# Kernel tuning notes

Hardware: AMD Instinct MI355X
Metric: run time of the kernel (lower is better)

Reference implementation:

```python
import jax, jax.numpy as jnp
import numpy as np

B, C, L, H, D = 2, 1024, 2048, 16, 64  # batch, n_factor, seq, heads, head_dim
LN_EPS = 1e-5


def setup_inputs() -> dict:
    key = jax.random.key(0)
    ks = jax.random.split(key, 8)
    s = 0.02
    return {
        "x": jax.random.normal(ks[0], (B, C, L), jnp.float32),
        "y": jax.random.normal(ks[1], (B, C, L), jnp.float32),
        "Wq": jax.random.normal(ks[2], (H, C, D), jnp.float32) * s,
        "Wk": jax.random.normal(ks[3], (H, C, D), jnp.float32) * s,
        "Wv": jax.random.normal(ks[4], (H, C, D), jnp.float32) * s,
        "bq": jax.random.normal(ks[5], (H, D), jnp.float32) * s,
        "bk": jax.random.normal(ks[6], (H, D), jnp.float32) * s,
        "bv": jax.random.normal(ks[7], (H, D), jnp.float32) * s,
        "gamma": jnp.ones((C,), jnp.float32),
        "beta": jnp.zeros((C,), jnp.float32),
    }


def reference(x, y, Wq, Wk, Wv, bq, bk, bv, gamma, beta):
    # Per-head Conv1d(kernel=1) == per-position linear; batch all heads at once.
    # x,y: [B, C, L]; W*: [H, C, D]; result q/k/v: [B, H, L, D]
    q = jnp.einsum('bcl,hcd->bhld', x, Wq) + bq[None, :, None, :]
    k = jnp.einsum('bcl,hcd->bhld', y, Wk) + bk[None, :, None, :]
    v = jnp.einsum('bcl,hcd->bhld', y, Wv) + bv[None, :, None, :]

    scale = 1.0 / jnp.sqrt(jnp.float32(D))  # n_factor_head ** 0.5
    scores = jnp.einsum('bhqd,bhkd->bhqk', q, k) * scale  # [B,H,L,L]
    attn = jax.nn.softmax(scores, axis=-1)
    ctx = jnp.einsum('bhqk,bhkd->bhqd', attn, v)  # [B,H,L,D]

    # torch.cat over heads along last dim == [B, L, H*D]
    att = jnp.transpose(ctx, (0, 2, 1, 3)).reshape(B, L, H * D)

    h = jnp.transpose(x, (0, 2, 1)) + att  # residual on x permuted to [B,L,C]
    mu = jnp.mean(h, axis=-1, keepdims=True)
    var = jnp.var(h, axis=-1, keepdims=True)
    out = (h - mu) * jax.lax.rsqrt(var + LN_EPS) * gamma + beta
    # dropout: identity in eval mode
    return out
```

## Files before the change

### kernel.cpp

```cpp
#include <hip/hip_runtime.h>
#include <hip/hip_bf16.h>

#define DEVI __device__ __forceinline__

typedef unsigned short u16;
typedef __bf16 bf16x8 __attribute__((ext_vector_type(8)));
typedef float f32x4 __attribute__((ext_vector_type(4)));

constexpr int Bn = 2, Cn = 1024, Ln = 2048, Hn = 16, Dn = 64;

DEVI u16 f2bfu(float f) { return __builtin_bit_cast(u16, __float2bfloat16(f)); }
DEVI float bfu2f(u16 u) { return __bfloat162float(__builtin_bit_cast(__hip_bfloat16, u)); }
DEVI f32x4 mfma16(bf16x8 a, bf16x8 b, f32x4 c) {
  return __builtin_amdgcn_mfma_f32_16x16x32_bf16(a, b, c, 0, 0, 0);
}
DEVI unsigned pk2(float lo, float hi) {
  return (unsigned)f2bfu(lo) | ((unsigned)f2bfu(hi) << 16);
}
DEVI void gld16(const u16* g, u16* l) {
  __builtin_amdgcn_global_load_lds(
      (const __attribute__((address_space(1))) unsigned*)g,
      (__attribute__((address_space(3))) unsigned*)l, 16, 0, 0);
}
DEVI int fsw(int row) { return (row & 7) ^ (((row >> 3) & 1) << 2); }

__global__ __launch_bounds__(256) void transpose_xy(const float* __restrict__ x,
                                                    const float* __restrict__ y,
                                                    u16* __restrict__ xT,
                                                    u16* __restrict__ yT) {
  int z = blockIdx.z;
  int which = z >> 1, b = z & 1;
  const float* src = (which ? y : x) + (size_t)b * Cn * Ln;
  u16* dst = (which ? yT : xT) + (size_t)b * Ln * Cn;
  int l0 = blockIdx.x * 64, c0 = blockIdx.y * 64;
  __shared__ float tile[64][65];
  int t = threadIdx.x;
  #pragma unroll
  for (int i = 0; i < 16; ++i) {
    int idx = i * 256 + t;
    int r = idx >> 6, cc = idx & 63;
    tile[r][cc] = src[(size_t)(c0 + r) * Ln + (l0 + cc)];
  }
  __syncthreads();
  #pragma unroll
  for (int i = 0; i < 8; ++i) {
    int idx = i * 256 + t;
    int r = idx >> 5, cc = (idx & 31) * 2;
    unsigned pkv = pk2(tile[cc][r], tile[cc + 1][r]);
    *(unsigned*)(&dst[(size_t)(l0 + r) * Cn + (c0 + cc)]) = pkv;
  }
}

__global__ __launch_bounds__(256) void transpose_w(const float* __restrict__ Wq,
                                                   const float* __restrict__ Wk,
                                                   const float* __restrict__ Wv,
                                                   u16* __restrict__ WT) {
  int c0 = blockIdx.x * 64, h = blockIdx.y, which = blockIdx.z;
  const float* src = (which == 0 ? Wq : (which == 1 ? Wk : Wv)) + (size_t)h * Cn * Dn;
  u16* dst = WT + ((size_t)which * Hn + h) * Dn * Cn;
  __shared__ float tile[64][65];
  int t = threadIdx.x;
  #pragma unroll
  for (int i = 0; i < 16; ++i) {
    int idx = i * 256 + t;
    int r = idx >> 6, cc = idx & 63;
    tile[r][cc] = src[(size_t)(c0 + r) * Dn + cc];
  }
  __syncthreads();
  #pragma unroll
  for (int i = 0; i < 16; ++i) {
    int idx = i * 256 + t;
    int r = idx >> 6, cc = idx & 63;
    dst[(size_t)r * Cn + (c0 + cc)] = f2bfu(tile[cc][r]);
  }
}

__global__ __launch_bounds__(512, 2) void gemm256(const u16* __restrict__ xT,
                                                  const u16* __restrict__ yT,
                                                  const u16* __restrict__ WT,
                                                  const float* __restrict__ bq,
                                                  const float* __restrict__ bk,
                                                  const float* __restrict__ bv,
                                                  u16* __restrict__ Qb,
                                                  u16* __restrict__ Kb,
                                                  u16* __restrict__ Vt) {
  int mt = blockIdx.x, by = blockIdx.y;
  int which = by >> 2, hp = by & 3;
  int b = mt >> 3, l0 = (mt & 7) * 256;
  const u16* A = (which == 0 ? xT : yT) + (size_t)mt * 256 * Cn;
  const u16* Bw = WT + ((size_t)which * 1024 + (size_t)hp * 256) * Cn;
  __shared__ __align__(16) u16 smem[4 * 256 * 64];
  int t = threadIdx.x, wave = t >> 6, lane = t & 63;
  int wr = wave >> 2, wc = wave & 3;
  int ml = lane & 15, kg = lane >> 4;
  f32x4 acc[8][4] = {};

  auto stage = [&](int buf, int k0) {
    u16* la = smem + buf * 16384;
    u16* lb = smem + 32768 + buf * 16384;
    #pragma unroll
    for (int j = 0; j < 4; ++j) {
      int slot = j * 512 + t;
      int row = slot >> 3, p = slot & 7, c16 = p ^ (row & 7);
      gld16(A + (size_t)row * Cn + k0 + c16 * 8, la + (j * 512 + wave * 64) * 8);
    }
    #pragma unroll
    for (int j = 0; j < 4; ++j) {
      int slot = j * 512 + t;
      int row = slot >> 3, p = slot & 7, c16 = p ^ (row & 7);
      gld16(Bw + (size_t)row * Cn + k0 + c16 * 8, lb + (j * 512 + wave * 64) * 8);
    }
  };

  stage(0, 0);
  stage(1, 64);
  asm volatile("s_waitcnt vmcnt(8)" ::: "memory");
  __builtin_amdgcn_s_barrier();
  __builtin_amdgcn_sched_barrier(0);

  constexpr int NK = Cn / 64;
  for (int tk = 0; tk < NK; ++tk) {
    int cur = tk & 1;
    if (tk >= 1) {
      if (tk + 1 < NK) {
        stage(cur ^ 1, (tk + 1) * 64);
        asm volatile("s_waitcnt vmcnt(8)" ::: "memory");
      } else {
        asm volatile("s_waitcnt vmcnt(0)" ::: "memory");
      }
      __builtin_amdgcn_s_barrier();
      __builtin_amdgcn_sched_barrier(0);
    }
    const u16* La = smem + cur * 16384;
    const u16* Lb = smem + 32768 + cur * 16384;
    bf16x8 bf[4][2];
    #pragma unroll
    for (int n = 0; n < 4; ++n) {
      int row = wc * 64 + n * 16 + ml;
      #pragma unroll
      for (int kk = 0; kk < 2; ++kk) {
        int p = (kk * 4 + kg) ^ (row & 7);
        bf[n][kk] = *(const bf16x8*)(&Lb[row * 64 + p * 8]);
      }
    }
    #pragma unroll
    for (int mq = 0; mq < 4; ++mq) {
      bf16x8 af[2][2];
      #pragma unroll
      for (int m2 = 0; m2 < 2; ++m2) {
        int row = wr * 128 + mq * 32 + m2 * 16 + ml;
        #pragma unroll
        for (int kk = 0; kk < 2; ++kk) {
          int p = (kk * 4 + kg) ^ (row & 7);
          af[m2][kk] = *(const bf16x8*)(&La[row * 64 + p * 8]);
        }
      }
      __builtin_amdgcn_s_setprio(1);
      #pragma unroll
      for (int m2 = 0; m2 < 2; ++m2)
        #pragma unroll
        for (int n = 0; n < 4; ++n)
          #pragma unroll
          for (int kk = 0; kk < 2; ++kk)
            acc[mq * 2 + m2][n] = mfma16(af[m2][kk], bf[n][kk], acc[mq * 2 + m2][n]);
      __builtin_amdgcn_s_setprio(0);
    }
    asm volatile("s_waitcnt lgkmcnt(0)" ::: "memory");
    __builtin_amdgcn_s_barrier();
  }

  int head = hp * 4 + wc;
  const float* bp = (which == 0 ? bq : (which == 1 ? bk : bv));
  if (which < 2) {
    u16* O = (which == 0 ? Qb : Kb) + (((size_t)b * Hn + head) * Ln + l0) * Dn;
    #pragma unroll
    for (int n = 0; n < 4; ++n) {
      float bvv = bp[head * 64 + n * 16 + ml];
      #pragma unroll
      for (int m = 0; m < 8; ++m)
        #pragma unroll
        for (int r = 0; r < 4; ++r) {
          int row = wr * 128 + m * 16 + kg * 4 + r;
          O[(size_t)row * Dn + n * 16 + ml] = f2bfu(acc[m][n][r] + bvv);
        }
    }
  } else {
    __syncthreads();
    #pragma unroll
    for (int n = 0; n < 4; ++n) {
      float bvv = bp[head * 64 + n * 16 + ml];
      int n_loc = wc * 64 + n * 16 + ml;
      int swz = (n_loc & 7) << 4;
      #pragma unroll
      for (int m = 0; m < 8; ++m) {
        int l_base = wr * 128 + m * 16 + kg * 4;
        uint2 pkd;
        pkd.x = pk2(acc[m][n][0] + bvv, acc[m][n][1] + bvv);
        pkd.y = pk2(acc[m][n][2] + bvv, acc[m][n][3] + bvv);
        *(uint2*)(&smem[n_loc * 256 + (l_base ^ swz)]) = pkd;
      }
    }
    __syncthreads();
    u16* Vbase = Vt + (((size_t)b * Hn + hp * 4) * Dn) * Ln + l0;
    #pragma unroll
    for (int j = 0; j < 16; ++j) {
      int chunk = j * 512 + t;
      int n = chunk >> 5, lc = chunk & 31;
      uint4 vv = *(const uint4*)(&smem[n * 256 + ((lc * 8) ^ ((n & 7) << 4))]);
      *(uint4*)(Vbase + (size_t)n * Ln + lc * 8) = vv;
    }
  }
}

__global__ __launch_bounds__(256, 4) void flash_attn(const u16* __restrict__ Qg,
                                                     const u16* __restrict__ Kg,
                                                     const u16* __restrict__ Vtg,
                                                     u16* __restrict__ att) {
  int n = blockIdx.x + 32 * (blockIdx.y + 16 * blockIdx.z);
  int xcd = n & 7, m = n >> 3;
  int grp = xcd * 4 + (m >> 5);
  int qt = m & 31;
  int h = grp & 15, b = grp >> 4;

  size_t bh = (size_t)b * Hn + h;
  const u16* Qp = Qg + (bh * Ln + (size_t)qt * 64) * Dn;
  const u16* Kp = Kg + bh * Ln * Dn;
  const u16* Vp = Vtg + bh * Dn * Ln;
  int t = threadIdx.x, wave = t >> 6, lane = t & 63;
  int qs = wave & 1, g = wave >> 1;
  int ml = lane & 15, kg = lane >> 4;
  __shared__ __align__(16) u16 Kl[2][64 * 64];
  __shared__ __align__(16) u16 Vl[2][64 * 64];

  constexpr float QS = 0.125f * 1.44269504f;
  bf16x8 qf[2][2];
  #pragma unroll
  for (int qg = 0; qg < 2; ++qg)
    #pragma unroll
    for (int kk = 0; kk < 2; ++kk) {
      bf16x8 raw = *(const bf16x8*)(Qp + (size_t)(qs * 32 + qg * 16 + ml) * Dn + kk * 32 + kg * 8);
      #pragma unroll
      for (int j = 0; j < 8; ++j) raw[j] = (__bf16)((float)raw[j] * QS);
      qf[qg][kk] = raw;
    }

  f32x4 ctx[2][4] = {};
  float psum[2] = {0.f, 0.f};

  int koff[2][2], voff[4];
  {
    #pragma unroll
    for (int nt = 0; nt < 2; ++nt) {
      int rowk = g * 32 + 8 * (ml >> 2) + 4 * nt + (ml & 3);
      #pragma unroll
      for (int kk = 0; kk < 2; ++kk)
        koff[nt][kk] = rowk * 64 + (((kk * 4 + kg) ^ fsw(rowk)) << 3);
    }
    #pragma unroll
    for (int nt = 0; nt < 4; ++nt) {
      int rowv = nt * 16 + ml;
      voff[nt] = rowv * 64 + ((((g * 4 + kg) ^ fsw(rowv))) << 3);
    }
  }
  int row_st[2], c16_st[2];
  #pragma unroll
  for (int j = 0; j < 2; ++j) {
    int q = j * 256 + t;
    row_st[j] = q >> 3;
    c16_st[j] = ((q & 7) ^ fsw(row_st[j])) * 8;
  }

  auto stage = [&](int buf, int kv0) {
    #pragma unroll
    for (int j = 0; j < 2; ++j)
      gld16(Kp + (size_t)(kv0 + row_st[j]) * Dn + c16_st[j],
            &Kl[buf][(j * 256 + wave * 64) * 8]);
    #pragma unroll
    for (int j = 0; j < 2; ++j)
      gld16(Vp + (size_t)row_st[j] * Ln + kv0 + c16_st[j],
            &Vl[buf][(j * 256 + wave * 64) * 8]);
  };

  constexpr int NT = Ln / 64;

  auto tile = [&](int cur, int tt) {
    if (tt + 1 < NT) {
      stage(cur ^ 1, (tt + 1) * 64);
      asm volatile("s_waitcnt vmcnt(4)" ::: "memory");
    } else {
      asm volatile("s_waitcnt vmcnt(0)" ::: "memory");
    }
    __builtin_amdgcn_s_barrier();
    __builtin_amdgcn_sched_barrier(0);
    const u16* Kh = Kl[cur];
    const u16* Vh = Vl[cur];
    bf16x8 kf[2][2];
    #pragma unroll
    for (int nt = 0; nt < 2; ++nt)
      #pragma unroll
      for (int kk = 0; kk < 2; ++kk)
        kf[nt][kk] = *(const bf16x8*)(&Kh[koff[nt][kk]]);
    f32x4 s[2][2] = {};
    __builtin_amdgcn_s_setprio(1);
    #pragma unroll
    for (int nt = 0; nt < 2; ++nt)
      #pragma unroll
      for (int kk = 0; kk < 2; ++kk)
        #pragma unroll
        for (int qg = 0; qg < 2; ++qg)
          s[qg][nt] = mfma16(kf[nt][kk], qf[qg][kk], s[qg][nt]);
    __builtin_amdgcn_s_setprio(0);
    bf16x8 pf[2];
    #pragma unroll
    for (int qg = 0; qg < 2; ++qg) {
      f32x4 e0, e1;
      #pragma unroll
      for (int r = 0; r < 4; ++r) e0[r] = __builtin_amdgcn_exp2f(s[qg][0][r]);
      #pragma unroll
      for (int r = 0; r < 4; ++r) e1[r] = __builtin_amdgcn_exp2f(s[qg][1][r]);
      psum[qg] += (e0[0] + e0[1]) + (e0[2] + e0[3]) + (e1[0] + e1[1]) + (e1[2] + e1[3]);
      uint4 pw;
      pw.x = pk2(e0[0], e0[1]);
      pw.y = pk2(e0[2], e0[3]);
      pw.z = pk2(e1[0], e1[1]);
      pw.w = pk2(e1[2], e1[3]);
      pf[qg] = __builtin_bit_cast(bf16x8, pw);
    }
    __builtin_amdgcn_s_setprio(1);
    #pragma unroll
    for (int nt = 0; nt < 4; ++nt) {
      bf16x8 vf = *(const bf16x8*)(&Vh[voff[nt]]);
      #pragma unroll
      for (int qg = 0; qg < 2; ++qg)
        ctx[qg][nt] = mfma16(pf[qg], vf, ctx[qg][nt]);
    }
    __builtin_amdgcn_s_setprio(0);
    asm volatile("s_waitcnt lgkmcnt(0)" ::: "memory");
    __builtin_amdgcn_s_barrier();
  };

  stage(0, 0);
  asm volatile("s_waitcnt vmcnt(0)" ::: "memory");
  __builtin_amdgcn_s_barrier();

  for (int tt = 0; tt < NT; tt += 2) {
    tile(0, tt);
    tile(1, tt + 1);
  }

  __syncthreads();
  float* comb = (float*)&Kl[0][0];
  float* psA = (float*)&Vl[0][0];
  if (g == 1) {
    #pragma unroll
    for (int qg = 0; qg < 2; ++qg) {
      #pragma unroll
      for (int nt = 0; nt < 4; ++nt)
        #pragma unroll
        for (int r = 0; r < 4; ++r)
          comb[(((qs * 2 + qg) * 16) + nt * 4 + r) * 64 + lane] = ctx[qg][nt][r];
      psA[(qs * 2 + qg) * 64 + lane] = psum[qg];
    }
  }
  __syncthreads();
  if (g == 0) {
    #pragma unroll
    for (int qg = 0; qg < 2; ++qg) {
      #pragma unroll
      for (int nt = 0; nt < 4; ++nt)
        #pragma unroll
        for (int r = 0; r < 4; ++r)
          ctx[qg][nt][r] += comb[(((qs * 2 + qg) * 16) + nt * 4 + r) * 64 + lane];
      psum[qg] += psA[(qs * 2 + qg) * 64 + lane];
      psum[qg] += __shfl_xor(psum[qg], 16);
      psum[qg] += __shfl_xor(psum[qg], 32);
    }
    #pragma unroll
    for (int qg = 0; qg < 2; ++qg) {
      float inv[4];
      #pragma unroll
      for (int r = 0; r < 4; ++r) inv[r] = 1.f / __shfl(psum[qg], kg * 4 + r);
      #pragma unroll
      for (int nt = 0; nt < 4; ++nt)
        #pragma unroll
        for (int r = 0; r < 4; ++r) {
          size_t row = (size_t)b * Ln + qt * 64 + qs * 32 + qg * 16 + kg * 4 + r;
          att[row * Cn + h * Dn + nt * 16 + ml] = f2bfu(ctx[qg][nt][r] * inv[r]);
        }
    }
  }
}

__global__ __launch_bounds__(256) void ln_kernel(const u16* __restrict__ att,
                                                 const u16* __restrict__ xT,
                                                 const float* __restrict__ gamma,
                                                 const float* __restrict__ beta,
                                                 float* __restrict__ out) {
  size_t row = blockIdx.x;
  const u16* ap = att + row * Cn;
  const u16* xp = xT + row * Cn;
  float* op = out + row * Cn;
  int t = threadIdx.x;
  ushort4 a4 = *(const ushort4*)(ap + t * 4);
  ushort4 xv = *(const ushort4*)(xp + t * 4);
  float h0 = bfu2f(a4.x) + bfu2f(xv.x), h1 = bfu2f(a4.y) + bfu2f(xv.y);
  float h2 = bfu2f(a4.z) + bfu2f(xv.z), h3 = bfu2f(a4.w) + bfu2f(xv.w);
  float s = h0 + h1 + h2 + h3;
  float ss = h0 * h0 + h1 * h1 + h2 * h2 + h3 * h3;
  #pragma unroll
  for (int off = 1; off < 64; off <<= 1) {
    s += __shfl_xor(s, off);
    ss += __shfl_xor(ss, off);
  }
  __shared__ float red[8];
  int wave = t >> 6, lane = t & 63;
  if (lane == 0) { red[wave] = s; red[wave + 4] = ss; }
  __syncthreads();
  s = red[0] + red[1] + red[2] + red[3];
  ss = red[4] + red[5] + red[6] + red[7];
  float mu = s * (1.f / 1024.f);
  float var = ss * (1.f / 1024.f) - mu * mu;
  float rinv = rsqrtf(var + 1e-5f);
  float4 gmv = *(const float4*)(gamma + t * 4);
  float4 bev = *(const float4*)(beta + t * 4);
  float4 o;
  o.x = (h0 - mu) * rinv * gmv.x + bev.x;
  o.y = (h1 - mu) * rinv * gmv.y + bev.y;
  o.z = (h2 - mu) * rinv * gmv.z + bev.z;
  o.w = (h3 - mu) * rinv * gmv.w + bev.w;
  *(float4*)(op + t * 4) = o;
}

extern "C" void kernel_launch(void* const* d_in, const int* in_sizes, int n_in,
                              void* d_out, int out_size, void* d_ws, size_t ws_size,
                              hipStream_t stream) {
  const float* x = (const float*)d_in[0];
  const float* y = (const float*)d_in[1];
  const float* Wq = (const float*)d_in[2];
  const float* Wk = (const float*)d_in[3];
  const float* Wv = (const float*)d_in[4];
  const float* bq = (const float*)d_in[5];
  const float* bk = (const float*)d_in[6];
  const float* bv = (const float*)d_in[7];
  const float* gamma = (const float*)d_in[8];
  const float* beta = (const float*)d_in[9];
  float* out = (float*)d_out;

  char* ws = (char*)d_ws;
  u16* xT = (u16*)(ws + 0);
  u16* yT = (u16*)(ws + 8388608);
  u16* WT = (u16*)(ws + 16777216);
  u16* Qb = (u16*)(ws + 23068672);
  u16* Kb = (u16*)(ws + 31457280);
  u16* VT = (u16*)(ws + 39845888);
  u16* att = (u16*)(ws + 48234496);

  transpose_xy<<<dim3(Ln / 64, Cn / 64, 4), dim3(256), 0, stream>>>(x, y, xT, yT);
  transpose_w<<<dim3(Cn / 64, Hn, 3), dim3(256), 0, stream>>>(Wq, Wk, Wv, WT);
  gemm256<<<dim3(16, 12), dim3(512), 0, stream>>>(xT, yT, WT, bq, bk, bv, Qb, Kb, VT);
  flash_attn<<<dim3(Ln / 64, Hn, Bn), dim3(256), 0, stream>>>(Qb, Kb, VT, att);
  ln_kernel<<<dim3(Bn * Ln), dim3(256), 0, stream>>>(att, xT, gamma, beta, out);
}
```

Baseline: 104.6 us.

## Software-pipeline QK and PV across tiles with triple-buffered K/V

Restructures the flash attention loop so each phase computes QK^T for the current tile while doing exp and PV for the previous tile, using three LDS buffers for K and V. The aim is to overlap MFMA work with the exp/softmax dependency chain and keep loads further ahead. In exchange LDS use grows by half and launch bounds drop from 4 to 3 blocks per CU, which may reduce occupancy. The phase indexing and the tail handling (phase 31, with stage skipped at the end) have to line up with the buffer rotation to stay correct.

Result: slower. 294.5 us (+181.5%).

```diff
diff --git a/kernel.cpp b/kernel.cpp
--- a/kernel.cpp
+++ b/kernel.cpp
@@ -212,7 +212,7 @@
   }
 }
 
-__global__ __launch_bounds__(256, 4) void flash_attn(const u16* __restrict__ Qg,
+__global__ __launch_bounds__(256, 3) void flash_attn(const u16* __restrict__ Qg,
                                                      const u16* __restrict__ Kg,
                                                      const u16* __restrict__ Vtg,
                                                      u16* __restrict__ att) {
@@ -229,8 +229,8 @@
   int t = threadIdx.x, wave = t >> 6, lane = t & 63;
   int qs = wave & 1, g = wave >> 1;
   int ml = lane & 15, kg = lane >> 4;
-  __shared__ __align__(16) u16 Kl[2][64 * 64];
-  __shared__ __align__(16) u16 Vl[2][64 * 64];
+  __shared__ __align__(16) u16 Kl[3][64 * 64];
+  __shared__ __align__(16) u16 Vl[3][64 * 64];
 
   constexpr float QS = 0.125f * 1.44269504f;
   bf16x8 qf[2][2];
@@ -281,35 +281,26 @@
             &Vl[buf][(j * 256 + wave * 64) * 8]);
   };
 
-  constexpr int NT = Ln / 64;
-
-  auto tile = [&](int cur, int tt) {
-    if (tt + 1 < NT) {
-      stage(cur ^ 1, (tt + 1) * 64);
-      asm volatile("s_waitcnt vmcnt(4)" ::: "memory");
-    } else {
-      asm volatile("s_waitcnt vmcnt(0)" ::: "memory");
-    }
-    __builtin_amdgcn_s_barrier();
-    __builtin_amdgcn_sched_barrier(0);
-    const u16* Kh = Kl[cur];
-    const u16* Vh = Vl[cur];
+  auto QK = [&](const u16* Kh, f32x4 (&s)[2][2]) {
     bf16x8 kf[2][2];
     #pragma unroll
     for (int nt = 0; nt < 2; ++nt)
       #pragma unroll
       for (int kk = 0; kk < 2; ++kk)
         kf[nt][kk] = *(const bf16x8*)(&Kh[koff[nt][kk]]);
-    f32x4 s[2][2] = {};
     __builtin_amdgcn_s_setprio(1);
     #pragma unroll
     for (int nt = 0; nt < 2; ++nt)
       #pragma unroll
-      for (int kk = 0; kk < 2; ++kk)
-        #pragma unroll
-        for (int qg = 0; qg < 2; ++qg)
-          s[qg][nt] = mfma16(kf[nt][kk], qf[qg][kk], s[qg][nt]);
+      for (int qg = 0; qg < 2; ++qg) {
+        f32x4 z = {};
+        s[qg][nt] = mfma16(kf[nt][0], qf[qg][0], z);
+        s[qg][nt] = mfma16(kf[nt][1], qf[qg][1], s[qg][nt]);
+      }
     __builtin_amdgcn_s_setprio(0);
+  };
+
+  auto PVf = [&](const u16* Vh, f32x4 (&s)[2][2]) {
     bf16x8 pf[2];
     #pragma unroll
     for (int qg = 0; qg < 2; ++qg) {
@@ -335,18 +326,48 @@
         ctx[qg][nt] = mfma16(pf[qg], vf, ctx[qg][nt]);
     }
     __builtin_amdgcn_s_setprio(0);
+  };
+
+  constexpr int NT = Ln / 64;
+  f32x4 sA[2][2], sB[2][2];
+
+  auto phase = [&](int tt, const u16* Kh, const u16* VhPrev, int bufNext,
+                   f32x4 (&cur)[2][2], f32x4 (&prv)[2][2]) {
+    if (tt + 1 < NT) {
+      stage(bufNext, (tt + 1) * 64);
+      asm volatile("s_waitcnt vmcnt(4)" ::: "memory");
+    } else {
+      asm volatile("s_waitcnt vmcnt(0)" ::: "memory");
+    }
+    __builtin_amdgcn_s_barrier();
+    __builtin_amdgcn_sched_barrier(0);
+    QK(Kh, cur);
+    PVf(VhPrev, prv);
     asm volatile("s_waitcnt lgkmcnt(0)" ::: "memory");
     __builtin_amdgcn_s_barrier();
   };
 
   stage(0, 0);
-  asm volatile("s_waitcnt vmcnt(0)" ::: "memory");
+  stage(1, 64);
+  asm volatile("s_waitcnt vmcnt(4)" ::: "memory");
   __builtin_amdgcn_s_barrier();
-
-  for (int tt = 0; tt < NT; tt += 2) {
-    tile(0, tt);
-    tile(1, tt + 1);
-  }
+  __builtin_amdgcn_sched_barrier(0);
+  QK(&Kl[0][0], sA);
+  asm volatile("s_waitcnt lgkmcnt(0)" ::: "memory");
+  __builtin_amdgcn_s_barrier();
+
+  for (int i = 0; i < 5; ++i) {
+    int tb = 1 + i * 6;
+    phase(tb + 0, &Kl[1][0], &Vl[0][0], 2, sB, sA);
+    phase(tb + 1, &Kl[2][0], &Vl[1][0], 0, sA, sB);
+    phase(tb + 2, &Kl[0][0], &Vl[2][0], 1, sB, sA);
+    phase(tb + 3, &Kl[1][0], &Vl[0][0], 2, sA, sB);
+    phase(tb + 4, &Kl[2][0], &Vl[1][0], 0, sB, sA);
+    phase(tb + 5, &Kl[0][0], &Vl[2][0], 1, sA, sB);
+  }
+
+  phase(31, &Kl[1][0], &Vl[0][0], 2 , sB, sA);
+  PVf(&Vl[1][0], sB);
 
   __syncthreads();
   float* comb = (float*)&Kl[0][0];
```
